# Kernel tuning notes

Hardware: AMD Instinct MI355X
Metric: run time of the kernel (lower is better)

Reference implementation:

```python
import jax, jax.numpy as jnp
import numpy as np

HIDDEN = 1024
HEADS = 16
HEAD_DIM = HIDDEN // HEADS


def setup_inputs() -> dict:
    key = jax.random.key(0)
    k1, k2, k3, k4, k5 = jax.random.split(key, 5)
    x = jax.random.normal(k1, (2, 4096, HIDDEN), dtype=jnp.float32)
    # torch nn.Linear params: weight [out, in], bias [out]
    s = 1.0 / np.sqrt(HIDDEN)
    qkv_w = jax.random.uniform(k2, (3 * HIDDEN, HIDDEN), jnp.float32, -s, s)
    qkv_b = jax.random.uniform(k3, (3 * HIDDEN,), jnp.float32, -s, s)
    out_w = jax.random.uniform(k4, (HIDDEN, HIDDEN), jnp.float32, -s, s)
    out_b = jax.random.uniform(k5, (HIDDEN,), jnp.float32, -s, s)
    return {"x": x, "qkv_w": qkv_w, "qkv_b": qkv_b, "out_w": out_w, "out_b": out_b}


def reference(x, qkv_w, qkv_b, out_w, out_b):
    B, N, C = x.shape
    qkv = x @ qkv_w.T + qkv_b  # [B, N, 3C]
    qkv = qkv.reshape(B, N, 3, HEADS, HEAD_DIM)
    qkv = jnp.transpose(qkv, (2, 0, 3, 1, 4))  # [3, B, H, N, D]
    q, k, v = qkv[0], qkv[1], qkv[2]
    scale = HEAD_DIM ** -0.5
    attn = jnp.einsum('bhnd,bhmd->bhnm', q, k) * scale
    attn = jax.nn.softmax(attn, axis=-1)
    out = jnp.einsum('bhnm,bhmd->bhnd', attn, v)  # [B, H, N, D]
    out = jnp.transpose(out, (0, 2, 1, 3)).reshape(B, N, C)
    return out @ out_w.T + out_b
```

## Files before the change

kernel.cpp:

```cpp
#include <hip/hip_runtime.h>
#include <hip/hip_bf16.h>

using bf16 = __hip_bfloat16;
typedef __attribute__((ext_vector_type(8))) short short8;
typedef __attribute__((ext_vector_type(4))) short short4v;
typedef __attribute__((ext_vector_type(4))) float floatx4;

#define MFMA16(a, b, c) __builtin_amdgcn_mfma_f32_16x16x32_bf16((a), (b), (c), 0, 0, 0)

constexpr int HID = 1024;
constexpr int NH = 16;
constexpr int HD = 64;
constexpr int NB = 2;
constexpr int SEQL = 4096;
#define QPRE 0.18033688011112042f

__device__ __forceinline__ short f32_to_bf16_bits(float p) {
    bf16 b = __float2bfloat16(p);
    short s;
    __builtin_memcpy(&s, &b, sizeof(s));
    return s;
}

__device__ __forceinline__ short8 cvt8(floatx4 a, floatx4 b) {
    short8 r;
#pragma unroll
    for (int i = 0; i < 4; ++i) {
        r[i]     = f32_to_bf16_bits(a[i]);
        r[i + 4] = f32_to_bf16_bits(b[i]);
    }
    return r;
}

__device__ __forceinline__ void gld16(const void* g, void* l) {
    __builtin_amdgcn_global_load_lds(
        (const __attribute__((address_space(1))) void*)g,
        (__attribute__((address_space(3))) void*)l, 16, 0, 0);
}


__global__ __launch_bounds__(256)
void cvt_pack(const float* __restrict__ in, short* __restrict__ out, int n8)
{
    const int i = blockIdx.x * 256 + threadIdx.x;
    if (i < n8) {
        const floatx4 a = ((const floatx4*)in)[2 * i];
        const floatx4 b = ((const floatx4*)in)[2 * i + 1];
        ((short8*)out)[i] = cvt8(a, b);
    }
}

template <int MODE>
__global__ __launch_bounds__(256)
void gemm_bt(const char* __restrict__ A_, const char* __restrict__ W,
             const float* __restrict__ bias, void* __restrict__ out0_,
             bf16* __restrict__ out1, bf16* __restrict__ out2, int nx)
{
    __shared__ __align__(16) short As[128 * 64];
    __shared__ __align__(16) short Bs[128 * 64];
    const int tid  = threadIdx.x;
    const int wave = tid >> 6;
    const int lane = tid & 63;
    const int quad = lane >> 4;
    const int l16  = lane & 15;
    const int sw   = l16 & 7;
    const int wm   = wave >> 1;
    const int wn   = wave & 1;

    const int bid  = blockIdx.x;
    const int cpx  = gridDim.x >> 3;
    const int swzb = (bid & 7) * cpx + (bid >> 3);
    const int m0   = (swzb / nx) * 128;
    const int n0   = (swzb % nx) * 128;

    const int lr   = lane >> 3;
    const int lcs  = (lane & 7) ^ (lr & 7);

    const char* ag = A_ + ((size_t)(m0 + wave * 32 + lr) * HID + lcs * 8) * 2;
    const char* bg = W  + ((size_t)(n0 + wave * 32 + lr) * HID + lcs * 8) * 2;
    const size_t row8 = (size_t)HID * 8 * 2;
    short* asw = As + (wave * 32) * 64;
    short* bsw = Bs + (wave * 32) * 64;

    floatx4 acc[4][4];
#pragma unroll
    for (int i = 0; i < 4; ++i)
#pragma unroll
        for (int j = 0; j < 4; ++j)
            acc[i][j] = (floatx4){0.f, 0.f, 0.f, 0.f};

    for (int k0 = 0; k0 < HID; k0 += 64) {
        __syncthreads();
#pragma unroll
        for (int i = 0; i < 4; ++i) {
            gld16(ag + (size_t)i * row8 + (size_t)k0 * 2, asw + i * 8 * 64);
            gld16(bg + (size_t)i * row8 + (size_t)k0 * 2, bsw + i * 8 * 64);
        }
        __syncthreads();
#pragma unroll
        for (int kk = 0; kk < 2; ++kk) {
            short8 af[4], bfr[4];
#pragma unroll
            for (int i = 0; i < 4; ++i) {
                af[i]  = *(const short8*)(As + (wm * 64 + i * 16 + l16) * 64 +
                                          (((kk * 4 + quad) ^ sw) * 8));
                bfr[i] = *(const short8*)(Bs + (wn * 64 + i * 16 + l16) * 64 +
                                          (((kk * 4 + quad) ^ sw) * 8));
            }
#pragma unroll
            for (int i = 0; i < 4; ++i)
#pragma unroll
                for (int j = 0; j < 4; ++j)
                    acc[i][j] = MFMA16(af[i], bfr[j], acc[i][j]);
        }
    }

#pragma unroll
    for (int j = 0; j < 4; ++j) {
        const int col = n0 + wn * 64 + j * 16 + l16;
        const float bv = bias[col];
        const int part = col >> 10;
        const int c = col & (HID - 1);
        const int h = c >> 6;
        const int d = c & 63;
#pragma unroll
        for (int i = 0; i < 4; ++i) {
            const int row0 = m0 + wm * 64 + i * 16 + quad * 4;
            if (MODE == 1 && part == 2) {
                const int b = row0 >> 12;
                const int npos0 = row0 & (SEQL - 1);
                const int nn = (npos0 >> 4) & 3;
                const int qq = (npos0 >> 2) & 3;
                const int nposP = (npos0 & ~63) | ((nn >> 1) << 5) | (qq << 3) |
                                  ((nn & 1) << 2);
                short4v pk;
#pragma unroll
                for (int r = 0; r < 4; ++r)
                    pk[r] = f32_to_bf16_bits(acc[i][j][r] + bv);
                *(short4v*)(out2 + ((size_t)(b * NH + h) * HD + d) * SEQL + nposP) = pk;
            } else {
#pragma unroll
                for (int r = 0; r < 4; ++r) {
                    const int row = row0 + r;
                    const float v = acc[i][j][r] + bv;
                    if (MODE == 0) {
                        ((float*)out0_)[(size_t)row * HID + col] = v;
                    } else {
                        const int b = row >> 12;
                        const int npos = row & (SEQL - 1);
                        const size_t bh = (size_t)(b * NH + h);
                        if (part == 0)
                            ((bf16*)out0_)[(bh * SEQL + npos) * HD + d] =
                                __float2bfloat16(v * QPRE);
                        else
                            out1[(bh * SEQL + npos) * HD + d] = __float2bfloat16(v);
                    }
                }
            }
        }
    }
}

__global__ __launch_bounds__(256, 2)
void flash_attn(const bf16* __restrict__ Qbf, const bf16* __restrict__ Kbf,
                const bf16* __restrict__ Vtbf, bf16* __restrict__ Og)
{
    __shared__ __align__(16) short Ks[2][64 * 64];
    __shared__ __align__(16) short Vs[2][64 * 64];
    const short* Qg = (const short*)Qbf;
    const int tid  = threadIdx.x;
    const int wave = tid >> 6;
    const int lane = tid & 63;
    const int quad = lane >> 4;
    const int l16  = lane & 15;
    const int sw   = l16 & 7;
    const int lr   = lane >> 3;
    const int lcs  = (lane & 7) ^ lr;
    const int bh   = blockIdx.y;
    const int q0   = blockIdx.x * 256;
    const size_t base = (size_t)bh * SEQL * HD;

    short8 qf[4][2];
#pragma unroll
    for (int mt = 0; mt < 4; ++mt) {
        const short* qp = Qg + base + (size_t)(q0 + wave * 64 + mt * 16 + l16) * HD + quad * 8;
        qf[mt][0] = *(const short8*)(qp);
        qf[mt][1] = *(const short8*)(qp + 32);
    }

    const char* kg = (const char*)Kbf + (base + (size_t)(wave * 16 + lr) * HD + lcs * 8) * 2;
    const char* vg = (const char*)Vtbf + (base + (size_t)(wave * 16 + lr) * SEQL + lcs * 8) * 2;

    auto stage = [&](int kt, short* ks, short* vs) {
        const char* k = kg + (size_t)kt * 64 * HD * 2;
        const char* v = vg + (size_t)kt * 64 * 2;
        short* kd = ks + (wave * 16) * 64;
        short* vd = vs + (wave * 16) * 64;
        gld16(k,                      kd);
        gld16(k + (size_t)8 * HD * 2, kd + 8 * 64);
        gld16(v,                        vd);
        gld16(v + (size_t)8 * SEQL * 2, vd + 8 * 64);
    };

    floatx4 oacc[4][4];
    floatx4 lacc[4];
#pragma unroll
    for (int mt = 0; mt < 4; ++mt) {
        lacc[mt] = (floatx4){0.f, 0.f, 0.f, 0.f};
#pragma unroll
        for (int dt = 0; dt < 4; ++dt) oacc[mt][dt] = (floatx4){0.f, 0.f, 0.f, 0.f};
    }

    const short8 ONESF = (short8)(short)0x3F80;

    auto compute = [&](const short* Kb, const short* Vb) {
        short8 kf[2][4];
#pragma unroll
        for (int n = 0; n < 4; ++n) {
            kf[0][n] = *(const short8*)(Kb + (n * 16 + l16) * 64 + ((quad ^ sw) * 8));
            kf[1][n] = *(const short8*)(Kb + (n * 16 + l16) * 64 + (((4 + quad) ^ sw) * 8));
        }
        short8 vf[2][4];
#pragma unroll
        for (int dt = 0; dt < 4; ++dt) {
            vf[0][dt] = *(const short8*)(Vb + (dt * 16 + l16) * 64 + ((quad ^ sw) * 8));
            vf[1][dt] = *(const short8*)(Vb + (dt * 16 + l16) * 64 + (((4 + quad) ^ sw) * 8));
        }

#pragma unroll
        for (int mt = 0; mt < 4; ++mt) {
            floatx4 s[4];
            __builtin_amdgcn_s_setprio(1);
#pragma unroll
            for (int n = 0; n < 4; ++n) {
                s[n] = (floatx4){0.f, 0.f, 0.f, 0.f};
                s[n] = MFMA16(kf[0][n], qf[mt][0], s[n]);
                s[n] = MFMA16(kf[1][n], qf[mt][1], s[n]);
            }
            __builtin_amdgcn_s_setprio(0);
            floatx4 pe[4];
#pragma unroll
            for (int n = 0; n < 4; ++n)
#pragma unroll
                for (int r = 0; r < 4; ++r)
                    pe[n][r] = __builtin_amdgcn_exp2f(s[n][r]);
            const short8 pa0 = cvt8(pe[0], pe[1]);
            const short8 pa1 = cvt8(pe[2], pe[3]);

            __builtin_amdgcn_s_setprio(1);
#pragma unroll
            for (int dt = 0; dt < 4; ++dt) {
                oacc[mt][dt] = MFMA16(pa0, vf[0][dt], oacc[mt][dt]);
                oacc[mt][dt] = MFMA16(pa1, vf[1][dt], oacc[mt][dt]);
            }
            lacc[mt] = MFMA16(pa0, ONESF, lacc[mt]);
            lacc[mt] = MFMA16(pa1, ONESF, lacc[mt]);
            __builtin_amdgcn_s_setprio(0);
        }
    };

    constexpr int NT = SEQL / 64;

    stage(0, Ks[0], Vs[0]);

    for (int kt = 0; kt < NT; kt += 2) {
        __syncthreads();
        if (kt + 1 < NT) stage(kt + 1, Ks[1], Vs[1]);
        compute(Ks[0], Vs[0]);

        __syncthreads();
        if (kt + 2 < NT) stage(kt + 2, Ks[0], Vs[0]);
        if (kt + 1 < NT) compute(Ks[1], Vs[1]);
    }

    const int b = bh >> 4;
    const int h = bh & 15;
#pragma unroll
    for (int mt = 0; mt < 4; ++mt) {
        floatx4 inv;
#pragma unroll
        for (int r = 0; r < 4; ++r) inv[r] = 1.0f / lacc[mt][r];
#pragma unroll
        for (int dt = 0; dt < 4; ++dt) {
#pragma unroll
            for (int r = 0; r < 4; ++r) {
                const int npos = q0 + wave * 64 + mt * 16 + quad * 4 + r;
                const int col = h * HD + dt * 16 + l16;
                Og[((size_t)(b * SEQL + npos)) * HID + col] =
                    __float2bfloat16(oacc[mt][dt][r] * inv[r]);
            }
        }
    }
}

extern "C" void kernel_launch(void* const* d_in, const int* in_sizes, int n_in,
                              void* d_out, int out_size, void* d_ws, size_t ws_size,
                              hipStream_t stream)
{
    const float* x     = (const float*)d_in[0];
    const float* qkv_w = (const float*)d_in[1];
    const float* qkv_b = (const float*)d_in[2];
    const float* out_w = (const float*)d_in[3];
    const float* out_b = (const float*)d_in[4];
    float* out = (float*)d_out;

    const size_t SZ = (size_t)NB * NH * SEQL * HD;
    bf16* q_ws  = (bf16*)d_ws;
    bf16* k_ws  = q_ws + SZ;
    bf16* vt_ws = k_ws + SZ;
    bf16* xb    = vt_ws + SZ;
    bf16* a_ws  = xb;
    bf16* wq    = xb + SZ;
    bf16* wo    = wq;

    dim3 blk(256);
    cvt_pack<<<dim3((NB * SEQL * HID) / 8 / 256), blk, 0, stream>>>(
        x, (short*)xb, NB * SEQL * HID / 8);
    cvt_pack<<<dim3((3 * HID * HID) / 8 / 256), blk, 0, stream>>>(
        qkv_w, (short*)wq, 3 * HID * HID / 8);

    {
        const int nx = 3 * HID / 128, ny = NB * SEQL / 128;
        gemm_bt<1><<<dim3(nx * ny), blk, 0, stream>>>(
            (const char*)xb, (const char*)wq, qkv_b, q_ws, k_ws, vt_ws, nx);
    }

    cvt_pack<<<dim3((HID * HID) / 8 / 256), blk, 0, stream>>>(
        out_w, (short*)wo, HID * HID / 8);

    flash_attn<<<dim3(SEQL / 256, NB * NH), dim3(256), 0, stream>>>(
        q_ws, k_ws, vt_ws, a_ws);

    {
        const int nx = HID / 128, ny = NB * SEQL / 128;
        gemm_bt<0><<<dim3(nx * ny), blk, 0, stream>>>(
            (const char*)a_ws, (const char*)wo, out_b, out, nullptr, nullptr, nx);
    }
}
```

Before: 304.2 us.

## Double-buffer GEMM shared-memory tiles with 32-wide K stages

Splits each 64-wide K step of the bf16 GEMM into two 32-wide stages held in two LDS buffers. The async global-to-LDS load of the next stage is issued before the MFMAs on the current stage, so load latency can overlap compute. The swizzle pattern is reworked for the 32-element row layout. Because the compiler may insert conservative vmcnt waits before the LDS reads, the overlap could be partly lost while the kernel still pays for extra barriers.

```diff
diff --git a/kernel.cpp b/kernel.cpp
--- a/kernel.cpp
+++ b/kernel.cpp
@@ -37,7 +37,6 @@
         (const __attribute__((address_space(1))) void*)g,
         (__attribute__((address_space(3))) void*)l, 16, 0, 0);
 }
-
 
 __global__ __launch_bounds__(256)
 void cvt_pack(const float* __restrict__ in, short* __restrict__ out, int n8)
@@ -56,14 +55,14 @@
              const float* __restrict__ bias, void* __restrict__ out0_,
              bf16* __restrict__ out1, bf16* __restrict__ out2, int nx)
 {
-    __shared__ __align__(16) short As[128 * 64];
-    __shared__ __align__(16) short Bs[128 * 64];
+    __shared__ __align__(16) short As[2][128 * 32];
+    __shared__ __align__(16) short Bs[2][128 * 32];
     const int tid  = threadIdx.x;
     const int wave = tid >> 6;
     const int lane = tid & 63;
     const int quad = lane >> 4;
     const int l16  = lane & 15;
-    const int sw   = l16 & 7;
+    const int skey = (l16 >> 1) & 3;
     const int wm   = wave >> 1;
     const int wn   = wave & 1;
 
@@ -73,14 +72,20 @@
     const int m0   = (swzb / nx) * 128;
     const int n0   = (swzb % nx) * 128;
 
-    const int lr   = lane >> 3;
-    const int lcs  = (lane & 7) ^ (lr & 7);
-
-    const char* ag = A_ + ((size_t)(m0 + wave * 32 + lr) * HID + lcs * 8) * 2;
-    const char* bg = W  + ((size_t)(n0 + wave * 32 + lr) * HID + lcs * 8) * 2;
-    const size_t row8 = (size_t)HID * 8 * 2;
-    short* asw = As + (wave * 32) * 64;
-    short* bsw = Bs + (wave * 32) * 64;
+    const int lr32 = lane >> 2;
+    const int lsrc = (lane & 3) ^ ((lane >> 3) & 3);
+    const char* ag = A_ + ((size_t)(m0 + wave * 32 + lr32) * HID + lsrc * 8) * 2;
+    const char* bg = W  + ((size_t)(n0 + wave * 32 + lr32) * HID + lsrc * 8) * 2;
+    const size_t row16 = (size_t)HID * 16 * 2;
+
+    auto stage = [&](int k0, int buf) {
+        short* ad = &As[buf][(wave * 32) * 32];
+        short* bd = &Bs[buf][(wave * 32) * 32];
+        gld16(ag + (size_t)k0 * 2,         ad);
+        gld16(ag + (size_t)k0 * 2 + row16, ad + 16 * 32);
+        gld16(bg + (size_t)k0 * 2,         bd);
+        gld16(bg + (size_t)k0 * 2 + row16, bd + 16 * 32);
+    };
 
     floatx4 acc[4][4];
 #pragma unroll
@@ -89,30 +94,30 @@
         for (int j = 0; j < 4; ++j)
             acc[i][j] = (floatx4){0.f, 0.f, 0.f, 0.f};
 
+    auto compute = [&](int buf) {
+        short8 af[4], bfr[4];
+#pragma unroll
+        for (int i = 0; i < 4; ++i) {
+            af[i]  = *(const short8*)(&As[buf][(wm * 64 + i * 16 + l16) * 32 +
+                                              ((quad ^ skey) * 8)]);
+            bfr[i] = *(const short8*)(&Bs[buf][(wn * 64 + i * 16 + l16) * 32 +
+                                              ((quad ^ skey) * 8)]);
+        }
+#pragma unroll
+        for (int i = 0; i < 4; ++i)
+#pragma unroll
+            for (int j = 0; j < 4; ++j)
+                acc[i][j] = MFMA16(af[i], bfr[j], acc[i][j]);
+    };
+
+    stage(0, 0);
     for (int k0 = 0; k0 < HID; k0 += 64) {
         __syncthreads();
-#pragma unroll
-        for (int i = 0; i < 4; ++i) {
-            gld16(ag + (size_t)i * row8 + (size_t)k0 * 2, asw + i * 8 * 64);
-            gld16(bg + (size_t)i * row8 + (size_t)k0 * 2, bsw + i * 8 * 64);
-        }
+        stage(k0 + 32, 1);
+        compute(0);
         __syncthreads();
-#pragma unroll
-        for (int kk = 0; kk < 2; ++kk) {
-            short8 af[4], bfr[4];
-#pragma unroll
-            for (int i = 0; i < 4; ++i) {
-                af[i]  = *(const short8*)(As + (wm * 64 + i * 16 + l16) * 64 +
-                                          (((kk * 4 + quad) ^ sw) * 8));
-                bfr[i] = *(const short8*)(Bs + (wn * 64 + i * 16 + l16) * 64 +
-                                          (((kk * 4 + quad) ^ sw) * 8));
-            }
-#pragma unroll
-            for (int i = 0; i < 4; ++i)
-#pragma unroll
-                for (int j = 0; j < 4; ++j)
-                    acc[i][j] = MFMA16(af[i], bfr[j], acc[i][j]);
-        }
+        if (k0 + 64 < HID) stage(k0 + 64, 0);
+        compute(1);
     }
 
 #pragma unroll
```

Result: slower. 318.6 us (+4.7%).

## Add 256x256 double-buffered 8-wave GEMM for QKV projection

Applied to the files above, without the earlier changes.

Introduces gemm_8p, a 512-thread kernel with 256x256 output tiles, double-buffered LDS staging via global_load_lds interleaved with MFMA quarters, setprio around the MFMA bursts, and XCD-aware block swizzling. It is used for the QKV projection only. The epilogue is factored into a shared helper. The larger tiles raise reuse and overlap loads with compute, at the cost of 128KB of LDS, high register pressure, and fewer blocks (384) for the grid.

```diff
diff --git a/kernel.cpp b/kernel.cpp
--- a/kernel.cpp
+++ b/kernel.cpp
@@ -38,7 +38,6 @@
         (__attribute__((address_space(3))) void*)l, 16, 0, 0);
 }
 
-
 __global__ __launch_bounds__(256)
 void cvt_pack(const float* __restrict__ in, short* __restrict__ out, int n8)
 {
@@ -47,6 +46,162 @@
         const floatx4 a = ((const floatx4*)in)[2 * i];
         const floatx4 b = ((const floatx4*)in)[2 * i + 1];
         ((short8*)out)[i] = cvt8(a, b);
+    }
+}
+
+template <int MODE>
+__device__ __forceinline__ void epi_store(
+    const floatx4& a4, int row0, int col, float bv,
+    void* __restrict__ out0_, bf16* __restrict__ out1, bf16* __restrict__ out2)
+{
+    const int part = col >> 10;
+    const int c = col & (HID - 1);
+    const int h = c >> 6;
+    const int d = c & 63;
+    if (MODE == 1 && part == 2) {
+        const int b = row0 >> 12;
+        const int npos0 = row0 & (SEQL - 1);
+        const int nn = (npos0 >> 4) & 3;
+        const int qq = (npos0 >> 2) & 3;
+        const int nposP = (npos0 & ~63) | ((nn >> 1) << 5) | (qq << 3) |
+                          ((nn & 1) << 2);
+        short4v pk;
+#pragma unroll
+        for (int r = 0; r < 4; ++r)
+            pk[r] = f32_to_bf16_bits(a4[r] + bv);
+        *(short4v*)(out2 + ((size_t)(b * NH + h) * HD + d) * SEQL + nposP) = pk;
+    } else {
+#pragma unroll
+        for (int r = 0; r < 4; ++r) {
+            const int row = row0 + r;
+            const float v = a4[r] + bv;
+            if (MODE == 0) {
+                ((float*)out0_)[(size_t)row * HID + col] = v;
+            } else {
+                const int b = row >> 12;
+                const int npos = row & (SEQL - 1);
+                const size_t bh = (size_t)(b * NH + h);
+                if (part == 0)
+                    ((bf16*)out0_)[(bh * SEQL + npos) * HD + d] =
+                        __float2bfloat16(v * QPRE);
+                else
+                    out1[(bh * SEQL + npos) * HD + d] = __float2bfloat16(v);
+            }
+        }
+    }
+}
+
+template <int MODE>
+__global__ __launch_bounds__(512, 2)
+void gemm_8p(const char* __restrict__ A_, const char* __restrict__ W,
+             const float* __restrict__ bias, void* __restrict__ out0_,
+             bf16* __restrict__ out1, bf16* __restrict__ out2, int nx)
+{
+    __shared__ __align__(16) short As[2][256 * 64];
+    __shared__ __align__(16) short Bs[2][256 * 64];
+    const int tid  = threadIdx.x;
+    const int wave = tid >> 6;
+    const int lane = tid & 63;
+    const int quad = lane >> 4;
+    const int l16  = lane & 15;
+    const int sw   = l16 & 7;
+    const int wm   = wave >> 2;
+    const int wn   = wave & 3;
+
+    const int bid  = blockIdx.x;
+    const int cpx  = gridDim.x >> 3;
+    const int swzb = (bid & 7) * cpx + (bid >> 3);
+    const int m0   = (swzb / nx) * 256;
+    const int n0   = (swzb % nx) * 256;
+
+    const int lr   = lane >> 3;
+    const int lcs  = (lane & 7) ^ (lr & 7);
+    const char* ag = A_ + ((size_t)(m0 + wave * 32 + lr) * HID + lcs * 8) * 2;
+    const char* bg = W  + ((size_t)(n0 + wave * 32 + lr) * HID + lcs * 8) * 2;
+    const size_t row8 = (size_t)HID * 8 * 2;
+
+    floatx4 acc[8][4];
+#pragma unroll
+    for (int i = 0; i < 8; ++i)
+#pragma unroll
+        for (int j = 0; j < 4; ++j)
+            acc[i][j] = (floatx4){0.f, 0.f, 0.f, 0.f};
+
+    auto stageA = [&](int k0, int buf, int u) {
+#pragma unroll
+        for (int i = 2 * u; i < 2 * u + 2; ++i)
+            gld16(ag + (size_t)i * row8 + (size_t)k0 * 2,
+                  &As[buf][(wave * 32 + i * 8) * 64]);
+    };
+    auto stageB = [&](int k0, int buf, int u) {
+#pragma unroll
+        for (int i = 2 * u; i < 2 * u + 2; ++i)
+            gld16(bg + (size_t)i * row8 + (size_t)k0 * 2,
+                  &Bs[buf][(wave * 32 + i * 8) * 64]);
+    };
+
+    constexpr int KT = HID / 64;
+
+    stageA(0, 0, 0); stageA(0, 0, 1);
+    stageB(0, 0, 0); stageB(0, 0, 1);
+    asm volatile("s_waitcnt vmcnt(0)" ::: "memory");
+    __builtin_amdgcn_s_barrier();
+
+    for (int kt = 0; kt < KT; ++kt) {
+        const int p    = kt & 1;
+        const int kn   = (kt + 1) * 64;
+        const bool more = (kt + 1 < KT);
+#pragma unroll
+        for (int q = 0; q < 4; ++q) {
+            const int qi = q >> 1, qj = q & 1;
+            short8 af[4][2], bf[2][2];
+#pragma unroll
+            for (int i4 = 0; i4 < 4; ++i4)
+#pragma unroll
+                for (int kk = 0; kk < 2; ++kk)
+                    af[i4][kk] = *(const short8*)(
+                        &As[p][(wm * 128 + (qi * 4 + i4) * 16 + l16) * 64 +
+                               (((kk * 4 + quad) ^ sw) * 8)]);
+#pragma unroll
+            for (int j2 = 0; j2 < 2; ++j2)
+#pragma unroll
+                for (int kk = 0; kk < 2; ++kk)
+                    bf[j2][kk] = *(const short8*)(
+                        &Bs[p][(wn * 64 + (qj * 2 + j2) * 16 + l16) * 64 +
+                               (((kk * 4 + quad) ^ sw) * 8)]);
+            if (more) {
+                if (q == 0)      { stageA(kn, 1 - p, 0); stageA(kn, 1 - p, 1); }
+                else if (q == 1) { stageB(kn, 1 - p, 0); stageB(kn, 1 - p, 1); }
+            }
+            __builtin_amdgcn_s_barrier();
+            __builtin_amdgcn_s_setprio(1);
+#pragma unroll
+            for (int i4 = 0; i4 < 4; ++i4)
+#pragma unroll
+                for (int j2 = 0; j2 < 2; ++j2)
+#pragma unroll
+                    for (int kk = 0; kk < 2; ++kk)
+                        acc[qi * 4 + i4][qj * 2 + j2] =
+                            MFMA16(af[i4][kk], bf[j2][kk],
+                                   acc[qi * 4 + i4][qj * 2 + j2]);
+            __builtin_amdgcn_s_setprio(0);
+            if (q == 3) {
+                asm volatile("s_waitcnt vmcnt(0)" ::: "memory");
+            }
+            __builtin_amdgcn_s_barrier();
+            if (q == 3) __builtin_amdgcn_sched_barrier(0);
+        }
+    }
+
+#pragma unroll
+    for (int j = 0; j < 4; ++j) {
+        const int col = n0 + wn * 64 + j * 16 + l16;
+        const float bv = bias[col];
+#pragma unroll
+        for (int i = 0; i < 8; ++i) {
+            const int row0 = m0 + wm * 128 + i * 16 + quad * 4;
+            epi_store<MODE>(acc[i][j], row0, col, bv, out0_, out1, out2);
+        }
     }
 }
 
@@ -119,44 +274,10 @@
     for (int j = 0; j < 4; ++j) {
         const int col = n0 + wn * 64 + j * 16 + l16;
         const float bv = bias[col];
-        const int part = col >> 10;
-        const int c = col & (HID - 1);
-        const int h = c >> 6;
-        const int d = c & 63;
 #pragma unroll
         for (int i = 0; i < 4; ++i) {
             const int row0 = m0 + wm * 64 + i * 16 + quad * 4;
-            if (MODE == 1 && part == 2) {
-                const int b = row0 >> 12;
-                const int npos0 = row0 & (SEQL - 1);
-                const int nn = (npos0 >> 4) & 3;
-                const int qq = (npos0 >> 2) & 3;
-                const int nposP = (npos0 & ~63) | ((nn >> 1) << 5) | (qq << 3) |
-                                  ((nn & 1) << 2);
-                short4v pk;
-#pragma unroll
-                for (int r = 0; r < 4; ++r)
-                    pk[r] = f32_to_bf16_bits(acc[i][j][r] + bv);
-                *(short4v*)(out2 + ((size_t)(b * NH + h) * HD + d) * SEQL + nposP) = pk;
-            } else {
-#pragma unroll
-                for (int r = 0; r < 4; ++r) {
-                    const int row = row0 + r;
-                    const float v = acc[i][j][r] + bv;
-                    if (MODE == 0) {
-                        ((float*)out0_)[(size_t)row * HID + col] = v;
-                    } else {
-                        const int b = row >> 12;
-                        const int npos = row & (SEQL - 1);
-                        const size_t bh = (size_t)(b * NH + h);
-                        if (part == 0)
-                            ((bf16*)out0_)[(bh * SEQL + npos) * HD + d] =
-                                __float2bfloat16(v * QPRE);
-                        else
-                            out1[(bh * SEQL + npos) * HD + d] = __float2bfloat16(v);
-                    }
-                }
-            }
+            epi_store<MODE>(acc[i][j], row0, col, bv, out0_, out1, out2);
         }
     }
 }
@@ -320,8 +441,8 @@
         qkv_w, (short*)wq, 3 * HID * HID / 8);
 
     {
-        const int nx = 3 * HID / 128, ny = NB * SEQL / 128;
-        gemm_bt<1><<<dim3(nx * ny), blk, 0, stream>>>(
+        const int nx = 3 * HID / 256, ny = NB * SEQL / 256;
+        gemm_8p<1><<<dim3(nx * ny), dim3(512), 0, stream>>>(
             (const char*)xb, (const char*)wq, qkv_b, q_ws, k_ws, vt_ws, nx);
     }
 
```

New measurement: 319.5 us. +5.0%, slower.
